# Performance work log

Measured on AMD Instinct MI355X. Metric: run time of the kernel, lower is better.

Reference implementation:

```python
import jax, jax.numpy as jnp
import numpy as np

TOP_K = 2  # num_active_experts


def setup_inputs() -> dict:
    key = jax.random.key(0)
    k1, k2, k3 = jax.random.split(key, 3)
    N, D, E = 16384, 1024, 8
    x = jax.random.normal(k1, (N, D), dtype=jnp.float32)
    router_w = jax.random.normal(k2, (E, D), dtype=jnp.float32) * (1.0 / np.sqrt(D))
    router_b = jnp.zeros((E,), dtype=jnp.float32)
    expert_w = jax.random.normal(k3, (E, D, D), dtype=jnp.float32) * (1.0 / np.sqrt(D))
    expert_b = jnp.zeros((E, D), dtype=jnp.float32)
    return {"x": x, "router_w": router_w, "router_b": router_b,
            "expert_w": expert_w, "expert_b": expert_b}


def reference(x, router_w, router_b, expert_w, expert_b):
    E = router_w.shape[0]
    # Router: softmax over experts, pick top-k, renormalize
    logits = x @ router_w.T + router_b                      # [N, E]
    probs = jax.nn.softmax(logits, axis=-1)                 # [N, E]
    top_p, top_i = jax.lax.top_k(probs, TOP_K)              # [N, K]
    top_p = top_p / jnp.sum(top_p, axis=-1, keepdims=True)  # renormalized gates
    # Dense combine weights: [N, E], zero for non-selected experts
    combine = jnp.sum(jax.nn.one_hot(top_i, E, dtype=x.dtype) * top_p[..., None], axis=1)
    # All-expert outputs, then weighted combine (vectorized dispatch/combine)
    y = jnp.einsum('nd,eod->neo', x, expert_w) + expert_b   # [N, E, O]
    out = jnp.einsum('neo,ne->no', y, combine)              # [N, O]
    return out
```

## Files before the change

kernel.cpp:

```cpp
#include <hip/hip_runtime.h>
#include <hip/hip_bf16.h>


constexpr int DIMS = 1024;
constexpr int NE   = 8;
constexpr int ROUTER_BLOCKS = 1024;
constexpr int WCONV_BLOCKS  = NE * DIMS * DIMS / (8 * 256);

typedef __attribute__((ext_vector_type(8))) short short8;
typedef __attribute__((ext_vector_type(4))) short short4_t;
typedef __attribute__((ext_vector_type(4))) float f32x4;

typedef const __attribute__((address_space(1))) void* gp_t;
typedef __attribute__((address_space(3))) void* sp_t;

__device__ __forceinline__ float b2f(unsigned short u) {
  union { unsigned int i; float f; } x; x.i = ((unsigned)u) << 16; return x.f;
}
__device__ __forceinline__ short f2bs(float f) {
  __hip_bfloat16 h = __float2bfloat16(f);
  return *(short*)&h;
}

__global__ __launch_bounds__(256) void prep_kernel(
    const float* __restrict__ x, const float* __restrict__ rw,
    const float* __restrict__ rb, const float* __restrict__ ew,
    __hip_bfloat16* __restrict__ xb, __hip_bfloat16* __restrict__ wb,
    int* __restrict__ counts, int* __restrict__ entries,
    float* __restrict__ gates, int n_tok) {
  const int tid = threadIdx.x;

  if ((int)blockIdx.x >= ROUTER_BLOCKS) {
    size_t i = (size_t)(blockIdx.x - ROUTER_BLOCKS) * 256 + tid;
    const float4* w4 = (const float4*)ew;
    float4 a = w4[i * 2], b = w4[i * 2 + 1];
    union { __hip_bfloat16 h[8]; float4 f; } u;
    u.h[0] = __float2bfloat16(a.x); u.h[1] = __float2bfloat16(a.y);
    u.h[2] = __float2bfloat16(a.z); u.h[3] = __float2bfloat16(a.w);
    u.h[4] = __float2bfloat16(b.x); u.h[5] = __float2bfloat16(b.y);
    u.h[6] = __float2bfloat16(b.z); u.h[7] = __float2bfloat16(b.w);
    ((float4*)wb)[i] = u.f;
    return;
  }

  __shared__ float s_rw[NE * DIMS];
  __shared__ int s_cnt[NE], s_base[NE];
  __shared__ int s_e[32];
  __shared__ float s_g[32];
  __shared__ int s_pos[32];

  const float4* rw4g = (const float4*)rw;
  float4* s4 = (float4*)s_rw;
  for (int i = tid; i < NE * DIMS / 4; i += 256) s4[i] = rw4g[i];
  if (tid < NE) s_cnt[tid] = 0;
  __syncthreads();

  const float4* s_rw4 = (const float4*)s_rw;
  const int wave = tid >> 6, lane = tid & 63;
  for (int i = 0; i < 4; ++i) {
    int t = blockIdx.x * 16 + wave * 4 + i;
    const float4* xr = (const float4*)(x + (size_t)t * DIMS);
    short4_t* xw = (short4_t*)(xb + (size_t)t * DIMS);
    float a[NE];
#pragma unroll
    for (int e = 0; e < NE; ++e) a[e] = 0.f;
#pragma unroll
    for (int j = 0; j < 4; ++j) {
      float4 v = xr[lane + j * 64];
      short4_t p;
      p[0] = f2bs(v.x); p[1] = f2bs(v.y); p[2] = f2bs(v.z); p[3] = f2bs(v.w);
      xw[lane + j * 64] = p;
#pragma unroll
      for (int e = 0; e < NE; ++e) {
        float4 w = s_rw4[e * 256 + lane + j * 64];
        a[e] = fmaf(v.x, w.x, fmaf(v.y, w.y, fmaf(v.z, w.z, fmaf(v.w, w.w, a[e]))));
      }
    }
#pragma unroll
    for (int off = 32; off > 0; off >>= 1) {
#pragma unroll
      for (int e = 0; e < NE; ++e) a[e] += __shfl_xor(a[e], off, 64);
    }
    if (lane == 0) {
      float l[NE];
#pragma unroll
      for (int e = 0; e < NE; ++e) l[e] = a[e] + rb[e];
      int e0 = 0;
#pragma unroll
      for (int e = 1; e < NE; ++e) if (l[e] > l[e0]) e0 = e;
      int e1 = (e0 == 0) ? 1 : 0;
#pragma unroll
      for (int e = 0; e < NE; ++e) if (e != e0 && l[e] > l[e1]) e1 = e;
      float r = expf(l[e1] - l[e0]);
      float g0 = 1.f / (1.f + r);
      float g1 = 1.f - g0;
      int ai = (wave * 4 + i) * 2;
      int p0 = atomicAdd(&s_cnt[e0], 1);
      int p1 = atomicAdd(&s_cnt[e1], 1);
      s_e[ai] = e0; s_g[ai] = g0; s_pos[ai] = p0;
      s_e[ai + 1] = e1; s_g[ai + 1] = g1; s_pos[ai + 1] = p1;
    }
  }
  __syncthreads();
  if (tid < NE) s_base[tid] = atomicAdd(&counts[tid], s_cnt[tid]);
  __syncthreads();
  if (tid < 32) {
    int e = s_e[tid];
    int p = s_base[e] + s_pos[tid];
    int tok = blockIdx.x * 16 + (tid >> 1);
    entries[e * n_tok + p] = (tok << 1) | (tid & 1);
    gates[e * n_tok + p] = s_g[tid];
  }
}

__global__ __launch_bounds__(256, 2) void moe_gemm(
    const __hip_bfloat16* __restrict__ xb, const __hip_bfloat16* __restrict__ wb,
    const float* __restrict__ eb, const int* __restrict__ counts,
    const int* __restrict__ entries, const float* __restrict__ gates,
    __hip_bfloat16* __restrict__ y, int n_tok) {
  int e = -1, rt = 0, cnt = 0, acc_t = 0;
#pragma unroll
  for (int i = 0; i < NE; ++i) {
    int c = counts[i];
    int t = (c + 255) >> 8;
    if (e < 0 && (int)blockIdx.y < acc_t + t) { e = i; rt = (int)blockIdx.y - acc_t; cnt = c; }
    acc_t += t;
  }
  if (e < 0) return;

  __shared__ __hip_bfloat16 As[256 * 32];
  __shared__ __hip_bfloat16 Bs[128 * 32];

  const int tid = threadIdx.x;
  const int lane = tid & 63, wave = tid >> 6;
  const int row0 = rt * 256;
  const int n0 = blockIdx.x * 128;

  const int srow = tid >> 2;
  const int kc = (tid & 3) ^ (srow & 3);
  const int kcol = kc * 8;

  const __hip_bfloat16* ap[4];
#pragma unroll
  for (int i = 0; i < 4; ++i) {
    int gr = row0 + srow + 64 * i;
    int ent = (gr < cnt) ? entries[e * n_tok + gr] : 0;
    ap[i] = xb + (size_t)(ent >> 1) * DIMS + kcol;
  }
  const __hip_bfloat16* wbase = wb + (size_t)e * DIMS * DIMS;
  const __hip_bfloat16* bp0 = wbase + (size_t)(n0 + srow) * DIMS + kcol;
  const __hip_bfloat16* bp1 = wbase + (size_t)(n0 + srow + 64) * DIMS + kcol;

  f32x4 acc[8][4] = {};

  const int wm = (wave & 1) * 128, wn = (wave >> 1) * 64;
  const int fr = lane & 15, quad = lane >> 4;
  const int swo = (quad ^ (fr & 3)) * 8;

  for (int k0 = 0; k0 < DIMS; k0 += 32) {
    __builtin_amdgcn_global_load_lds((gp_t)(ap[0] + k0), (sp_t)(As + tid * 8), 16, 0, 0);
    __builtin_amdgcn_global_load_lds((gp_t)(ap[1] + k0), (sp_t)(As + (tid + 256) * 8), 16, 0, 0);
    __builtin_amdgcn_global_load_lds((gp_t)(ap[2] + k0), (sp_t)(As + (tid + 512) * 8), 16, 0, 0);
    __builtin_amdgcn_global_load_lds((gp_t)(ap[3] + k0), (sp_t)(As + (tid + 768) * 8), 16, 0, 0);
    __builtin_amdgcn_global_load_lds((gp_t)(bp0 + k0), (sp_t)(Bs + tid * 8), 16, 0, 0);
    __builtin_amdgcn_global_load_lds((gp_t)(bp1 + k0), (sp_t)(Bs + (tid + 256) * 8), 16, 0, 0);
    __syncthreads();
    short8 af[8], bf[4];
#pragma unroll
    for (int mt = 0; mt < 8; ++mt)
      af[mt] = *(const short8*)&As[(wm + mt * 16 + fr) * 32 + swo];
#pragma unroll
    for (int nt = 0; nt < 4; ++nt)
      bf[nt] = *(const short8*)&Bs[(wn + nt * 16 + fr) * 32 + swo];
#pragma unroll
    for (int mt = 0; mt < 8; ++mt)
#pragma unroll
      for (int nt = 0; nt < 4; ++nt)
        acc[mt][nt] = __builtin_amdgcn_mfma_f32_16x16x32_bf16(af[mt], bf[nt], acc[mt][nt], 0, 0, 0);
    __syncthreads();
  }

  float bias[4];
#pragma unroll
  for (int nt = 0; nt < 4; ++nt) bias[nt] = eb[e * DIMS + n0 + wn + nt * 16 + fr];
#pragma unroll
  for (int mt = 0; mt < 8; ++mt) {
#pragma unroll
    for (int r = 0; r < 4; ++r) {
      int m = wm + mt * 16 + quad * 4 + r;
      int gr = row0 + m;
      if (gr < cnt) {
        int ent = entries[e * n_tok + gr];
        float g = gates[e * n_tok + gr];
        __hip_bfloat16* yp = y + (size_t)ent * DIMS + n0 + wn + fr;
#pragma unroll
        for (int nt = 0; nt < 4; ++nt)
          yp[nt * 16] = __float2bfloat16(g * (acc[mt][nt][r] + bias[nt]));
      }
    }
  }
}

__global__ __launch_bounds__(256) void combine_kernel(const __hip_bfloat16* __restrict__ y,
                                                      float* __restrict__ out) {
  size_t idx = (size_t)blockIdx.x * 256 + threadIdx.x;
  size_t n = idx >> 7;
  int c = (int)(idx & 127) << 3;
  short8 v0 = *(const short8*)(y + (n * 2) * DIMS + c);
  short8 v1 = *(const short8*)(y + (n * 2 + 1) * DIMS + c);
  float4 o0, o1;
  o0.x = b2f((unsigned short)v0[0]) + b2f((unsigned short)v1[0]);
  o0.y = b2f((unsigned short)v0[1]) + b2f((unsigned short)v1[1]);
  o0.z = b2f((unsigned short)v0[2]) + b2f((unsigned short)v1[2]);
  o0.w = b2f((unsigned short)v0[3]) + b2f((unsigned short)v1[3]);
  o1.x = b2f((unsigned short)v0[4]) + b2f((unsigned short)v1[4]);
  o1.y = b2f((unsigned short)v0[5]) + b2f((unsigned short)v1[5]);
  o1.z = b2f((unsigned short)v0[6]) + b2f((unsigned short)v1[6]);
  o1.w = b2f((unsigned short)v0[7]) + b2f((unsigned short)v1[7]);
  float* op = out + n * DIMS + c;
  ((float4*)op)[0] = o0;
  ((float4*)op)[1] = o1;
}

extern "C" void kernel_launch(void* const* d_in, const int* in_sizes, int n_in,
                              void* d_out, int out_size, void* d_ws, size_t ws_size,
                              hipStream_t stream) {
  const float* x  = (const float*)d_in[0];
  const float* rw = (const float*)d_in[1];
  const float* rb = (const float*)d_in[2];
  const float* ew = (const float*)d_in[3];
  const float* eb = (const float*)d_in[4];
  float* out = (float*)d_out;
  const int n_tok = in_sizes[0] / DIMS;

  char* ws = (char*)d_ws;
  size_t off = 0;
  int* counts = (int*)ws;                      off += 256;
  __hip_bfloat16* xb = (__hip_bfloat16*)(ws + off); off += (size_t)n_tok * DIMS * 2;
  __hip_bfloat16* wb = (__hip_bfloat16*)(ws + off); off += (size_t)NE * DIMS * DIMS * 2;
  int*   entries = (int*)(ws + off);           off += (size_t)NE * n_tok * 4;
  float* gates   = (float*)(ws + off);         off += (size_t)NE * n_tok * 4;
  __hip_bfloat16* y = (__hip_bfloat16*)(ws + off); off += (size_t)n_tok * 2 * DIMS * 2;
  if (ws_size < off) return;

  hipMemsetAsync(counts, 0, 256, stream);
  prep_kernel<<<ROUTER_BLOCKS + WCONV_BLOCKS, 256, 0, stream>>>(
      x, rw, rb, ew, xb, wb, counts, entries, gates, n_tok);
  dim3 g(DIMS / 128, 2 * n_tok / 256 + NE);
  moe_gemm<<<g, 256, 0, stream>>>(xb, wb, eb, counts, entries, gates, y, n_tok);
  combine_kernel<<<(unsigned)((size_t)n_tok * DIMS / 8 / 256), 256, 0, stream>>>(y, out);
}
```

Baseline: 301.8 us.

## Pre-swizzle expert weights into MFMA fragment layout and drop LDS staging

The weight conversion pass now writes bf16 expert weights in a layout that matches the MFMA B-fragment order, so each lane can load its fragment with one coalesced 16-byte global load. The GEMM drops the shared-memory tiles and barriers and reads A rows (gathered tokens) and B fragments straight from global memory into registers. The tile changes to 128 rows by 256 columns with a 64x128 per-wave tile. This removes LDS traffic and syncs, but gives up cross-wave operand sharing and leaves no explicit prefetch, so it depends on L2/L1 hit rates and on the compiler to hide load latency.

Result: slower. 321.2 us (+6.4%).

```diff
diff --git a/kernel.cpp b/kernel.cpp
--- a/kernel.cpp
+++ b/kernel.cpp
@@ -10,9 +10,6 @@
 typedef __attribute__((ext_vector_type(8))) short short8;
 typedef __attribute__((ext_vector_type(4))) short short4_t;
 typedef __attribute__((ext_vector_type(4))) float f32x4;
-
-typedef const __attribute__((address_space(1))) void* gp_t;
-typedef __attribute__((address_space(3))) void* sp_t;
 
 __device__ __forceinline__ float b2f(unsigned short u) {
   union { unsigned int i; float f; } x; x.i = ((unsigned)u) << 16; return x.f;
@@ -31,15 +28,21 @@
   const int tid = threadIdx.x;
 
   if ((int)blockIdx.x >= ROUTER_BLOCKS) {
-    size_t i = (size_t)(blockIdx.x - ROUTER_BLOCKS) * 256 + tid;
-    const float4* w4 = (const float4*)ew;
-    float4 a = w4[i * 2], b = w4[i * 2 + 1];
+    unsigned g = (unsigned)(blockIdx.x - ROUTER_BLOCKS) * 256 + tid;
+    int l  = g & 63;
+    int kc = (g >> 6) & 31;
+    int nb = (g >> 11) & 63;
+    int e  = g >> 17;
+    int row = nb * 16 + (l & 15);
+    int kb  = kc * 32 + ((l >> 4) << 3);
+    const float4* src = (const float4*)(ew + ((size_t)e << 20) + (size_t)row * DIMS + kb);
+    float4 a = src[0], b = src[1];
     union { __hip_bfloat16 h[8]; float4 f; } u;
     u.h[0] = __float2bfloat16(a.x); u.h[1] = __float2bfloat16(a.y);
     u.h[2] = __float2bfloat16(a.z); u.h[3] = __float2bfloat16(a.w);
     u.h[4] = __float2bfloat16(b.x); u.h[5] = __float2bfloat16(b.y);
     u.h[6] = __float2bfloat16(b.z); u.h[7] = __float2bfloat16(b.w);
-    ((float4*)wb)[i] = u.f;
+    ((float4*)wb)[g] = u.f;
     return;
   }
 
@@ -122,69 +125,51 @@
 #pragma unroll
   for (int i = 0; i < NE; ++i) {
     int c = counts[i];
-    int t = (c + 255) >> 8;
+    int t = (c + 127) >> 7;
     if (e < 0 && (int)blockIdx.y < acc_t + t) { e = i; rt = (int)blockIdx.y - acc_t; cnt = c; }
     acc_t += t;
   }
   if (e < 0) return;
 
-  __shared__ __hip_bfloat16 As[256 * 32];
-  __shared__ __hip_bfloat16 Bs[128 * 32];
-
   const int tid = threadIdx.x;
   const int lane = tid & 63, wave = tid >> 6;
-  const int row0 = rt * 256;
-  const int n0 = blockIdx.x * 128;
-
-  const int srow = tid >> 2;
-  const int kc = (tid & 3) ^ (srow & 3);
-  const int kcol = kc * 8;
-
-  const __hip_bfloat16* ap[4];
-#pragma unroll
-  for (int i = 0; i < 4; ++i) {
-    int gr = row0 + srow + 64 * i;
+  const int row0 = rt * 128;
+  const int n0 = blockIdx.x * 256;
+  const int wm = (wave & 1) * 64, wn = (wave >> 1) * 128;
+  const int fr = lane & 15, quad = lane >> 4;
+
+  const short8* ap[4];
+#pragma unroll
+  for (int mb = 0; mb < 4; ++mb) {
+    int gr = row0 + wm + mb * 16 + fr;
     int ent = (gr < cnt) ? entries[e * n_tok + gr] : 0;
-    ap[i] = xb + (size_t)(ent >> 1) * DIMS + kcol;
-  }
-  const __hip_bfloat16* wbase = wb + (size_t)e * DIMS * DIMS;
-  const __hip_bfloat16* bp0 = wbase + (size_t)(n0 + srow) * DIMS + kcol;
-  const __hip_bfloat16* bp1 = wbase + (size_t)(n0 + srow + 64) * DIMS + kcol;
-
-  f32x4 acc[8][4] = {};
-
-  const int wm = (wave & 1) * 128, wn = (wave >> 1) * 64;
-  const int fr = lane & 15, quad = lane >> 4;
-  const int swo = (quad ^ (fr & 3)) * 8;
-
-  for (int k0 = 0; k0 < DIMS; k0 += 32) {
-    __builtin_amdgcn_global_load_lds((gp_t)(ap[0] + k0), (sp_t)(As + tid * 8), 16, 0, 0);
-    __builtin_amdgcn_global_load_lds((gp_t)(ap[1] + k0), (sp_t)(As + (tid + 256) * 8), 16, 0, 0);
-    __builtin_amdgcn_global_load_lds((gp_t)(ap[2] + k0), (sp_t)(As + (tid + 512) * 8), 16, 0, 0);
-    __builtin_amdgcn_global_load_lds((gp_t)(ap[3] + k0), (sp_t)(As + (tid + 768) * 8), 16, 0, 0);
-    __builtin_amdgcn_global_load_lds((gp_t)(bp0 + k0), (sp_t)(Bs + tid * 8), 16, 0, 0);
-    __builtin_amdgcn_global_load_lds((gp_t)(bp1 + k0), (sp_t)(Bs + (tid + 256) * 8), 16, 0, 0);
-    __syncthreads();
-    short8 af[8], bf[4];
-#pragma unroll
-    for (int mt = 0; mt < 8; ++mt)
-      af[mt] = *(const short8*)&As[(wm + mt * 16 + fr) * 32 + swo];
-#pragma unroll
-    for (int nt = 0; nt < 4; ++nt)
-      bf[nt] = *(const short8*)&Bs[(wn + nt * 16 + fr) * 32 + swo];
-#pragma unroll
-    for (int mt = 0; mt < 8; ++mt)
-#pragma unroll
-      for (int nt = 0; nt < 4; ++nt)
+    ap[mb] = (const short8*)(xb + (size_t)(ent >> 1) * DIMS) + quad;
+  }
+
+  const short8* wb8 = (const short8*)wb;
+  const size_t bbase = ((((size_t)e * 64 + ((n0 + wn) >> 4)) * 32) << 6) + lane;
+
+  f32x4 acc[4][8] = {};
+
+#pragma unroll 2
+  for (int kc = 0; kc < 32; ++kc) {
+    short8 af[4], bf[8];
+#pragma unroll
+    for (int mb = 0; mb < 4; ++mb) af[mb] = ap[mb][kc * 4];
+#pragma unroll
+    for (int nt = 0; nt < 8; ++nt) bf[nt] = wb8[bbase + ((size_t)nt << 11) + (kc << 6)];
+#pragma unroll
+    for (int mt = 0; mt < 4; ++mt)
+#pragma unroll
+      for (int nt = 0; nt < 8; ++nt)
         acc[mt][nt] = __builtin_amdgcn_mfma_f32_16x16x32_bf16(af[mt], bf[nt], acc[mt][nt], 0, 0, 0);
-    __syncthreads();
-  }
-
-  float bias[4];
-#pragma unroll
-  for (int nt = 0; nt < 4; ++nt) bias[nt] = eb[e * DIMS + n0 + wn + nt * 16 + fr];
-#pragma unroll
-  for (int mt = 0; mt < 8; ++mt) {
+  }
+
+  float bias[8];
+#pragma unroll
+  for (int nt = 0; nt < 8; ++nt) bias[nt] = eb[e * DIMS + n0 + wn + nt * 16 + fr];
+#pragma unroll
+  for (int mt = 0; mt < 4; ++mt) {
 #pragma unroll
     for (int r = 0; r < 4; ++r) {
       int m = wm + mt * 16 + quad * 4 + r;
@@ -194,7 +179,7 @@
         float g = gates[e * n_tok + gr];
         __hip_bfloat16* yp = y + (size_t)ent * DIMS + n0 + wn + fr;
 #pragma unroll
-        for (int nt = 0; nt < 4; ++nt)
+        for (int nt = 0; nt < 8; ++nt)
           yp[nt * 16] = __float2bfloat16(g * (acc[mt][nt][r] + bias[nt]));
       }
     }
@@ -246,7 +231,7 @@
   hipMemsetAsync(counts, 0, 256, stream);
   prep_kernel<<<ROUTER_BLOCKS + WCONV_BLOCKS, 256, 0, stream>>>(
       x, rw, rb, ew, xb, wb, counts, entries, gates, n_tok);
-  dim3 g(DIMS / 128, 2 * n_tok / 256 + NE);
+  dim3 g(DIMS / 256, 2 * n_tok / 128 + NE);
   moe_gemm<<<g, 256, 0, stream>>>(xb, wb, eb, counts, entries, gates, y, n_tok);
   combine_kernel<<<(unsigned)((size_t)n_tok * DIMS / 8 / 256), 256, 0, stream>>>(y, out);
 }
```
